# Optimization experiments

Hardware: AMD Instinct MI355X
Metric: run time of the kernel (lower is better)

The kernel has to match this reference:

```python
import jax, jax.numpy as jnp
import numpy as np

B, N, M = 64, 1024, 1024
MAX_ITER = 10      # init default max_iter
EPS = 1e-4         # init default epsilon


def setup_inputs() -> dict:
    key = jax.random.key(0)
    k1, k2, k3 = jax.random.split(key, 3)
    s = jax.random.uniform(k1, (B, N, M), dtype=jnp.float32)
    # ragged valid sizes per batch element, in [N//2, N]
    nrows = jax.random.randint(k2, (B,), N // 2, N + 1, dtype=jnp.int32)
    ncols = jax.random.randint(k3, (B,), M // 2, M + 1, dtype=jnp.int32)
    return {"s": s, "nrows": nrows, "ncols": ncols}


def reference(s, nrows, ncols):
    # Faithful vectorized form of the torch loop:
    #   even iter: sum[b,i,j] = sum_{k<nrows[b]} s[b,k,j]  (masked column sums)
    #   odd  iter: sum[b,i,j] = sum_{k<ncols[b]} s[b,i,k]  (masked row sums)
    #   then s[b,i,j] *= 1/sum inside the [nrows[b], ncols[b]] block, 0 outside.
    Bb, Nn, Mm = s.shape
    row_mask = jnp.arange(Nn)[None, :] < nrows[:, None]          # [B, N]
    col_mask = jnp.arange(Mm)[None, :] < ncols[:, None]          # [B, M]
    block = row_mask[:, :, None] & col_mask[:, None, :]          # [B, N, M]

    s = s + jnp.float32(EPS)
    for i in range(MAX_ITER):
        if i % 2 == 0:
            # column normalization: sum over valid rows
            d = jnp.sum(jnp.where(row_mask[:, :, None], s, 0.0), axis=1, keepdims=True)  # [B,1,M]
            d = jnp.where(col_mask[:, None, :], d, 1.0)  # safe denom outside block
        else:
            # row normalization: sum over valid cols
            d = jnp.sum(jnp.where(col_mask[:, None, :], s, 0.0), axis=2, keepdims=True)  # [B,N,1]
            d = jnp.where(row_mask[:, :, None], d, 1.0)
        s = jnp.where(block, s / d, 0.0)
    return s
```

## Files before the change

kernel.cpp:

```cpp
#include <hip/hip_runtime.h>


#define BB 64
#define NN 1024
#define MM 1024
#define EPS 1e-4f

typedef _Float16 half_t;
typedef __attribute__((ext_vector_type(4))) _Float16 half4_t;
typedef __attribute__((ext_vector_type(8))) _Float16 half8_t;
typedef __attribute__((ext_vector_type(4))) float float4_t;

__global__ __launch_bounds__(256) void prep_kernel(
    const float* __restrict__ s, const int* __restrict__ nrows,
    const int* __restrict__ ncols, half_t* __restrict__ H,
    float* __restrict__ P) {
  int b = blockIdx.z, rc = blockIdx.y, stripe = blockIdx.x;
  int nr = nrows[b], nc = ncols[b];
  float* Pp = P + ((size_t)rc * BB + b) * MM + stripe * 128;
  if (stripe * 128 >= nc) {
    if (threadIdx.x < 128) Pp[threadIdx.x] = 0.f;
    return;
  }
  int tc = threadIdx.x & 31, tr = threadIdx.x >> 5;
  int j0 = stripe * 128 + tc * 4;
  const float* sp = s + (size_t)b * NN * MM + j0;
  half_t* hp = H + (size_t)b * NN * MM + j0;
  float4_t acc = {0.f, 0.f, 0.f, 0.f};
  int base = rc * 128;
#pragma unroll
  for (int it = 0; it < 16; it++) {
    int i = base + it * 8 + tr;
    if (i < nr) {
      float4_t v = *(const float4_t*)(sp + (size_t)i * MM);
      v.x += EPS; v.y += EPS; v.z += EPS; v.w += EPS;
      half4_t h = {(half_t)v.x, (half_t)v.y, (half_t)v.z, (half_t)v.w};
      *(half4_t*)(hp + (size_t)i * MM) = h;
      acc.x += v.x; acc.y += v.y; acc.z += v.z; acc.w += v.w;
    }
  }
  __shared__ float lds[8][128];
  *(float4_t*)&lds[tr][tc * 4] = acc;
  __syncthreads();
  if (threadIdx.x < 128) {
    float s0 = 0.f;
#pragma unroll
    for (int k = 0; k < 8; k++) s0 += lds[k][threadIdx.x];
    Pp[threadIdx.x] = s0;
  }
}

__global__ __launch_bounds__(256) void creduce_kernel(
    const float* __restrict__ P, const int* __restrict__ ncols,
    float* __restrict__ C) {
  int b = blockIdx.y;
  int j = blockIdx.x * 256 + threadIdx.x;
  int nc = ncols[b];
  float s0 = 0.f;
#pragma unroll
  for (int k = 0; k < 8; k++) s0 += P[((size_t)k * BB + b) * MM + j];
  C[b * MM + j] = (j < nc) ? 1.f / s0 : 0.f;
}

__global__ __launch_bounds__(256) void row_kernel(
    const half_t* __restrict__ H, const int* __restrict__ nrows,
    const int* __restrict__ ncols, const float* __restrict__ C,
    float* __restrict__ R) {
  int b = blockIdx.y;
  int nr = nrows[b], nc = ncols[b];
  int w = threadIdx.x >> 6, l = threadIdx.x & 63;
  int i = blockIdx.x * 4 + w;
  if (i >= nr) return;
  const half_t* hp = H + ((size_t)b * NN + i) * MM;
  const float* Cp = C + b * MM;
  float acc = 0.f;
#pragma unroll
  for (int ch = 0; ch < 2; ch++) {
    int base = ch * 512 + l * 8;
    if (base < nc) {
      half8_t h = *(const half8_t*)(hp + base);
      float4_t c0 = *(const float4_t*)(Cp + base);
      float4_t c1 = *(const float4_t*)(Cp + base + 4);
      acc += (float)h[0] * c0.x + (float)h[1] * c0.y + (float)h[2] * c0.z +
             (float)h[3] * c0.w + (float)h[4] * c1.x + (float)h[5] * c1.y +
             (float)h[6] * c1.z + (float)h[7] * c1.w;
    }
  }
#pragma unroll
  for (int off = 32; off > 0; off >>= 1) acc += __shfl_xor(acc, off, 64);
  if (l == 0) R[b * NN + i] = 1.f / acc;
}

__global__ __launch_bounds__(256) void col_kernel(
    const half_t* __restrict__ H, const int* __restrict__ nrows,
    const int* __restrict__ ncols, const float* __restrict__ R,
    float* __restrict__ P) {
  int b = blockIdx.z, rc = blockIdx.y, stripe = blockIdx.x;
  int nr = nrows[b], nc = ncols[b];
  float* Pp = P + ((size_t)rc * BB + b) * MM + stripe * 256;
  if (stripe * 256 >= nc) {
    Pp[threadIdx.x] = 0.f;
    return;
  }
  int tc = threadIdx.x & 31, tr = threadIdx.x >> 5;
  int j0 = stripe * 256 + tc * 8;
  const half_t* hp = H + (size_t)b * NN * MM + j0;
  const float* Rp = R + b * NN;
  float acc[8] = {0.f, 0.f, 0.f, 0.f, 0.f, 0.f, 0.f, 0.f};
  int base = rc * 128;
#pragma unroll
  for (int it = 0; it < 16; it++) {
    int i = base + it * 8 + tr;
    if (i < nr) {
      half8_t h = *(const half8_t*)(hp + (size_t)i * MM);
      float r = Rp[i];
#pragma unroll
      for (int k = 0; k < 8; k++) acc[k] += (float)h[k] * r;
    }
  }
  __shared__ float lds[8][256];
#pragma unroll
  for (int k = 0; k < 8; k++) lds[tr][tc * 8 + k] = acc[k];
  __syncthreads();
  float s0 = 0.f;
#pragma unroll
  for (int k = 0; k < 8; k++) s0 += lds[k][threadIdx.x];
  Pp[threadIdx.x] = s0;
}

__global__ __launch_bounds__(256) void final_kernel(
    const float* __restrict__ s, const int* __restrict__ nrows,
    const int* __restrict__ ncols, const float* __restrict__ C,
    float* __restrict__ out) {
  int b = blockIdx.y;
  int nr = nrows[b], nc = ncols[b];
  int w = threadIdx.x >> 6, l = threadIdx.x & 63;
  int i = blockIdx.x * 4 + w;
  float* op = out + ((size_t)b * NN + i) * MM;
  float4_t z = {0.f, 0.f, 0.f, 0.f};
  if (i >= nr) {
#pragma unroll
    for (int ch = 0; ch < 4; ch++) *(float4_t*)(op + ch * 256 + l * 4) = z;
    return;
  }
  const float* sp = s + ((size_t)b * NN + i) * MM;
  const float* Cp = C + b * MM;
  float4_t sv[4], cv[4];
  float acc = 0.f;
  int nch = (nc + 255) >> 8;
#pragma unroll
  for (int ch = 0; ch < 4; ch++) {
    if (ch < nch) {
      float4_t v = *(const float4_t*)(sp + ch * 256 + l * 4);
      v.x += EPS; v.y += EPS; v.z += EPS; v.w += EPS;
      sv[ch] = v;
      float4_t c = *(const float4_t*)(Cp + ch * 256 + l * 4);
      cv[ch] = c;
      acc += v.x * c.x + v.y * c.y + v.z * c.z + v.w * c.w;
    }
  }
#pragma unroll
  for (int off = 32; off > 0; off >>= 1) acc += __shfl_xor(acc, off, 64);
  float r = 1.f / acc;
#pragma unroll
  for (int ch = 0; ch < 4; ch++) {
    if (ch < nch) {
      float4_t o;
      o.x = sv[ch].x * cv[ch].x * r;
      o.y = sv[ch].y * cv[ch].y * r;
      o.z = sv[ch].z * cv[ch].z * r;
      o.w = sv[ch].w * cv[ch].w * r;
      *(float4_t*)(op + ch * 256 + l * 4) = o;
    } else {
      *(float4_t*)(op + ch * 256 + l * 4) = z;
    }
  }
}

extern "C" void kernel_launch(void* const* d_in, const int* in_sizes, int n_in,
                              void* d_out, int out_size, void* d_ws,
                              size_t ws_size, hipStream_t stream) {
  const float* s = (const float*)d_in[0];
  const int* nrows = (const int*)d_in[1];
  const int* ncols = (const int*)d_in[2];
  float* out = (float*)d_out;
  half_t* H = (half_t*)d_out;
  float* R = (float*)d_ws;
  float* C = R + BB * NN;
  float* P = C + BB * MM;

  dim3 pgrid(8, 8, BB);
  dim3 cgrid(4, 8, BB);
  dim3 rgrid(NN / 4, BB);
  dim3 dgrid(4, BB);

  prep_kernel<<<pgrid, 256, 0, stream>>>(s, nrows, ncols, H, P);
  creduce_kernel<<<dgrid, 256, 0, stream>>>(P, ncols, C);
  for (int t = 0; t < 4; t++) {
    row_kernel<<<rgrid, 256, 0, stream>>>(H, nrows, ncols, C, R);
    col_kernel<<<cgrid, 256, 0, stream>>>(H, nrows, ncols, R, P);
    creduce_kernel<<<dgrid, 256, 0, stream>>>(P, ncols, C);
  }
  final_kernel<<<rgrid, 256, 0, stream>>>(s, nrows, ncols, C, out);
}
```

Baseline: 597.8 us.

## Fuse column reduction into col_kernel and batch rows per wave in row_kernel

The column-sum kernel now has each block cover a full 64-column stripe across all rows and write reciprocal column factors directly. This removes the partial-sum buffer and the separate creduce launch on every iteration. The row kernel uses a smaller grid where each wave handles 8 rows and loads the column factors once. Together these cut launch count and workspace traffic, but col_kernel now runs only 16x64 blocks with a long serial row loop, which lowers parallelism and may leave the GPU underfilled.

Result: no change. 593.6 us (-0.7%).

```diff
diff --git a/kernel.cpp b/kernel.cpp
--- a/kernel.cpp
+++ b/kernel.cpp
@@ -68,49 +68,57 @@
     float* __restrict__ R) {
   int b = blockIdx.y;
   int nr = nrows[b], nc = ncols[b];
-  int w = threadIdx.x >> 6, l = threadIdx.x & 63;
-  int i = blockIdx.x * 4 + w;
-  if (i >= nr) return;
-  const half_t* hp = H + ((size_t)b * NN + i) * MM;
+  int l = threadIdx.x & 63;
+  int rg = blockIdx.x * 4 + (threadIdx.x >> 6);
   const float* Cp = C + b * MM;
-  float acc = 0.f;
-#pragma unroll
-  for (int ch = 0; ch < 2; ch++) {
-    int base = ch * 512 + l * 8;
-    if (base < nc) {
-      half8_t h = *(const half8_t*)(hp + base);
-      float4_t c0 = *(const float4_t*)(Cp + base);
-      float4_t c1 = *(const float4_t*)(Cp + base + 4);
-      acc += (float)h[0] * c0.x + (float)h[1] * c0.y + (float)h[2] * c0.z +
-             (float)h[3] * c0.w + (float)h[4] * c1.x + (float)h[5] * c1.y +
-             (float)h[6] * c1.z + (float)h[7] * c1.w;
-    }
-  }
-#pragma unroll
-  for (int off = 32; off > 0; off >>= 1) acc += __shfl_xor(acc, off, 64);
-  if (l == 0) R[b * NN + i] = 1.f / acc;
+  float4_t c00 = *(const float4_t*)(Cp + l * 8);
+  float4_t c01 = *(const float4_t*)(Cp + l * 8 + 4);
+  float4_t c10 = *(const float4_t*)(Cp + 512 + l * 8);
+  float4_t c11 = *(const float4_t*)(Cp + 512 + l * 8 + 4);
+  bool hi = (512 + l * 8) < nc;
+  const half_t* hp = H + (size_t)b * NN * MM + l * 8;
+#pragma unroll
+  for (int r = 0; r < 8; r++) {
+    int i = rg + (r << 7);
+    if (i < nr) {
+      const half_t* hr = hp + (size_t)i * MM;
+      half8_t h0 = *(const half8_t*)hr;
+      float acc = (float)h0[0] * c00.x + (float)h0[1] * c00.y +
+                  (float)h0[2] * c00.z + (float)h0[3] * c00.w +
+                  (float)h0[4] * c01.x + (float)h0[5] * c01.y +
+                  (float)h0[6] * c01.z + (float)h0[7] * c01.w;
+      if (hi) {
+        half8_t h1 = *(const half8_t*)(hr + 512);
+        acc += (float)h1[0] * c10.x + (float)h1[1] * c10.y +
+               (float)h1[2] * c10.z + (float)h1[3] * c10.w +
+               (float)h1[4] * c11.x + (float)h1[5] * c11.y +
+               (float)h1[6] * c11.z + (float)h1[7] * c11.w;
+      }
+#pragma unroll
+      for (int off = 32; off > 0; off >>= 1) acc += __shfl_xor(acc, off, 64);
+      if (l == 0) R[b * NN + i] = 1.f / acc;
+    }
+  }
 }
 
 __global__ __launch_bounds__(256) void col_kernel(
     const half_t* __restrict__ H, const int* __restrict__ nrows,
     const int* __restrict__ ncols, const float* __restrict__ R,
-    float* __restrict__ P) {
-  int b = blockIdx.z, rc = blockIdx.y, stripe = blockIdx.x;
-  int nr = nrows[b], nc = ncols[b];
-  float* Pp = P + ((size_t)rc * BB + b) * MM + stripe * 256;
-  if (stripe * 256 >= nc) {
-    Pp[threadIdx.x] = 0.f;
+    float* __restrict__ C) {
+  int b = blockIdx.y;
+  int j0 = blockIdx.x * 64;
+  int nr = nrows[b], nc = ncols[b];
+  if (j0 >= nc) {
+    if (threadIdx.x < 64) C[b * MM + j0 + threadIdx.x] = 0.f;
     return;
   }
-  int tc = threadIdx.x & 31, tr = threadIdx.x >> 5;
-  int j0 = stripe * 256 + tc * 8;
-  const half_t* hp = H + (size_t)b * NN * MM + j0;
+  int tc = threadIdx.x & 7, tr = threadIdx.x >> 3;
+  const half_t* hp = H + (size_t)b * NN * MM + j0 + tc * 8;
   const float* Rp = R + b * NN;
   float acc[8] = {0.f, 0.f, 0.f, 0.f, 0.f, 0.f, 0.f, 0.f};
-  int base = rc * 128;
-#pragma unroll
-  for (int it = 0; it < 16; it++) {
-    int i = base + it * 8 + tr;
+#pragma unroll 4
+  for (int it = 0; it < 32; it++) {
+    int i = (it << 5) + tr;
     if (i < nr) {
       half8_t h = *(const half8_t*)(hp + (size_t)i * MM);
       float r = Rp[i];
@@ -118,14 +126,17 @@
       for (int k = 0; k < 8; k++) acc[k] += (float)h[k] * r;
     }
   }
-  __shared__ float lds[8][256];
+  __shared__ float lds[32][64];
 #pragma unroll
   for (int k = 0; k < 8; k++) lds[tr][tc * 8 + k] = acc[k];
   __syncthreads();
-  float s0 = 0.f;
-#pragma unroll
-  for (int k = 0; k < 8; k++) s0 += lds[k][threadIdx.x];
-  Pp[threadIdx.x] = s0;
+  if (threadIdx.x < 64) {
+    float s0 = 0.f;
+#pragma unroll
+    for (int k = 0; k < 32; k++) s0 += lds[k][threadIdx.x];
+    int j = j0 + threadIdx.x;
+    C[b * MM + j] = (j < nc) ? 1.f / s0 : 0.f;
+  }
 }
 
 __global__ __launch_bounds__(256) void final_kernel(
@@ -190,16 +201,16 @@
   float* P = C + BB * MM;
 
   dim3 pgrid(8, 8, BB);
-  dim3 cgrid(4, 8, BB);
-  dim3 rgrid(NN / 4, BB);
   dim3 dgrid(4, BB);
+  dim3 rgrid(32, BB);
+  dim3 cgrid(16, BB);
+  dim3 fgrid(NN / 4, BB);
 
   prep_kernel<<<pgrid, 256, 0, stream>>>(s, nrows, ncols, H, P);
   creduce_kernel<<<dgrid, 256, 0, stream>>>(P, ncols, C);
   for (int t = 0; t < 4; t++) {
     row_kernel<<<rgrid, 256, 0, stream>>>(H, nrows, ncols, C, R);
-    col_kernel<<<cgrid, 256, 0, stream>>>(H, nrows, ncols, R, P);
-    creduce_kernel<<<dgrid, 256, 0, stream>>>(P, ncols, C);
-  }
-  final_kernel<<<rgrid, 256, 0, stream>>>(s, nrows, ncols, C, out);
-}
+    col_kernel<<<cgrid, 256, 0, stream>>>(H, nrows, ncols, R, C);
+  }
+  final_kernel<<<fgrid, 256, 0, stream>>>(s, nrows, ncols, C, out);
+}
```
